# Kernel tuning notes

Measured on AMD Instinct MI355X. Metric: run time of the kernel, lower is better.

Reference implementation:

```python
import jax, jax.numpy as jnp
import numpy as np

N = 200_000      # active voxels
C_IN = 128
C_OUT = 128
GRID = 128
K = 27           # 3x3x3 submanifold kernel offsets
EPS = 1e-4       # scn BatchNormalization default eps
LEAK = 0.333     # scn LeakyReLU default leakiness


def _build_neighbor_idx(rng):
    # unique active voxel coords via unique linear keys in GRID^3
    keys = rng.choice(GRID ** 3, size=N, replace=False).astype(np.int64)
    z = keys % GRID
    y = (keys // GRID) % GRID
    x = keys // (GRID * GRID)
    coords = np.stack([x, y, z], axis=1)  # [N,3]
    order = np.argsort(keys)
    sorted_keys = keys[order]
    offs = np.array([(dx, dy, dz) for dx in (-1, 0, 1)
                     for dy in (-1, 0, 1) for dz in (-1, 0, 1)], dtype=np.int64)
    nb = np.full((N, K), -1, dtype=np.int32)
    for k in range(K):
        q = coords + offs[k]  # [N,3]
        inb = np.all((q >= 0) & (q < GRID), axis=1)
        qk = (q[:, 0] * GRID + q[:, 1]) * GRID + q[:, 2]
        pos = np.searchsorted(sorted_keys, qk)
        pos = np.clip(pos, 0, N - 1)
        hit = inb & (sorted_keys[pos] == qk)
        nb[:, k] = np.where(hit, order[pos].astype(np.int32), -1)
    return nb


def setup_inputs() -> dict:
    key = jax.random.key(0)
    k1, k2 = jax.random.split(key)
    rng = np.random.default_rng(0)
    neighbor_idx = jnp.asarray(_build_neighbor_idx(rng))       # [N,27] int32, -1 = inactive
    features = jax.random.normal(k1, (N, C_IN), dtype=jnp.float32)
    # per-offset conv weights, scn-style init scale
    W = jax.random.normal(k2, (K, C_IN, C_OUT), dtype=jnp.float32) * (1.0 / np.sqrt(K * C_IN))
    b = jnp.zeros((C_OUT,), dtype=jnp.float32)
    gamma = jnp.ones((C_OUT,), dtype=jnp.float32)
    beta = jnp.zeros((C_OUT,), dtype=jnp.float32)
    return {"features": features, "W": W, "b": b, "gamma": gamma,
            "beta": beta, "neighbor_idx": neighbor_idx}


def reference(features, W, b, gamma, beta, neighbor_idx):
    # Submanifold 3D conv: output only at active sites; gather active neighbors.
    valid = (neighbor_idx >= 0)                      # [N,27] bool
    idx = jnp.where(valid, neighbor_idx, 0)          # safe gather index
    out = jnp.broadcast_to(b, (features.shape[0], C_OUT))
    for k in range(K):  # fixed structural loop over 27 kernel offsets
        xk = features[idx[:, k]] * valid[:, k:k + 1].astype(features.dtype)  # [N,C_IN]
        out = out + xk @ W[k]                                                # [N,C_OUT]
    # BatchNormalization over all active sites (training-mode batch stats)
    mean = jnp.mean(out, axis=0)
    var = jnp.var(out, axis=0)
    out = (out - mean) * jax.lax.rsqrt(var + EPS) * gamma + beta
    # LeakyReLU (scn default leakiness 0.333)
    return jnp.where(out > 0, out, LEAK * out)
```

## Files before the change

### kernel.cpp

```cpp
#include <hip/hip_runtime.h>
#include <hip/hip_bf16.h>

#define N_VOX 200000
#define CI 128
#define CO 128
#define KK 27
#define BM 96
#define NBLK96 2084
#define NBLKFB 1563
#define NSTEP 54
#define LEAK 0.333f
#define BN_EPS 1e-4f
#define SENT 0x3FFFFu
#define ACC_STRIDE 132
#define RB_CAP 48

typedef unsigned short u16;
typedef unsigned int u32;
typedef __attribute__((ext_vector_type(8))) short short8;
typedef __attribute__((ext_vector_type(4))) float f32x4;

typedef const __attribute__((address_space(1))) u32* gptr_t;
typedef __attribute__((address_space(3))) u32* lptr_t;

__device__ __forceinline__ u16 f2bf(float f) {
  union { float f; u32 u; } x; x.f = f;
  return (u16)((x.u + 0x7FFFu + ((x.u >> 16) & 1u)) >> 16);
}
__device__ __forceinline__ u16 cvt_bf(float f) {
  union { __hip_bfloat16 h; u16 u; } c;
  c.h = __float2bfloat16(f);
  return c.u;
}
__device__ __forceinline__ int kbase_of(int k) {
  return (k < 13) ? k * RB_CAP : (k == 13 ? 13 * RB_CAP : 13 * RB_CAP + 96 + (k - 14) * RB_CAP);
}

__global__ __launch_bounds__(256) void fcast_kernel(const float* __restrict__ f,
                                                    u16* __restrict__ fb) {
  size_t i = ((size_t)blockIdx.x * 256 + threadIdx.x) * 8;
  float4 a = *(const float4*)(f + i);
  float4 b = *(const float4*)(f + i + 4);
  u16 t[8];
  t[0] = cvt_bf(a.x); t[1] = cvt_bf(a.y); t[2] = cvt_bf(a.z); t[3] = cvt_bf(a.w);
  t[4] = cvt_bf(b.x); t[5] = cvt_bf(b.y); t[6] = cvt_bf(b.z); t[7] = cvt_bf(b.w);
  *(uint4*)(fb + i) = *(const uint4*)t;
}

__global__ __launch_bounds__(256) void wcast3_kernel(const float* __restrict__ W,
                                                     u16* __restrict__ Wt3) {
  int gid = blockIdx.x * 256 + threadIdx.x;
  int lane = gid & 63, chunk = gid >> 6;
  int ks = chunk & 3, nf = (chunk >> 2) & 7, k = chunk >> 5;
  int lr = lane & 15, lg = lane >> 4;
  int co = nf * 16 + lr;
  int ci0 = ks * 32 + lg * 8;
  const float* Wk = W + (size_t)k * CI * CO;
  u16 t[8];
#pragma unroll
  for (int e = 0; e < 8; ++e) t[e] = f2bf(Wk[(ci0 + e) * CO + co]);
  *(uint4*)(Wt3 + (size_t)gid * 8) = *(const uint4*)t;
}

__global__ __launch_bounds__(256, 2) void conv_sp_kernel(
    const u16* __restrict__ featb, const u16* __restrict__ Wt3,
    const int* __restrict__ nb, const u16* __restrict__ zp,
    float* __restrict__ out, float* __restrict__ partial) {
  __shared__ __align__(16) char smem[73088];
  float* const accf = (float*)smem;
  u16* const ring = (u16*)(smem + 50688);
  u32* const rb_lds = (u32*)(smem + 67072);
  int* const cnt_lds = (int*)(smem + 72448);
  int* const wcnt = (int*)(smem + 72560);
  u32* const wl = (u32*)(smem + 72576);
  int* const wl_n = (int*)(smem + 72960);
  float* const ps = (float*)smem;

  const int tid = threadIdx.x;
  const int bid = blockIdx.x;
  const int row0 = bid * BM;
  const int lane = tid & 63;
  const int w = tid >> 6;

  {
    f32x4 z4 = {0.f, 0.f, 0.f, 0.f};
    for (int i = tid; i < (BM * ACC_STRIDE) / 4; i += 256) ((f32x4*)accf)[i] = z4;
  }

  {
    const bool inrow = (tid < BM) && (row0 + tid < N_VOX);
    const int* nbp = nb + (size_t)(row0 + tid) * KK;
    int vv[KK];
#pragma unroll
    for (int k = 0; k < KK; ++k) vv[k] = (k != 13 && inrow) ? nbp[k] : -1;
    if (tid < BM)
      rb_lds[13 * RB_CAP + tid] = ((u32)tid << 18) | (inrow ? (u32)(row0 + tid) : SENT);
    if (tid == 0) cnt_lds[13] = BM;
#pragma unroll
    for (int k = 0; k < KK; ++k) {
      if (k == 13) continue;
      bool valid = vv[k] >= 0;
      unsigned long long m = __ballot(valid);
      if (lane == 0) wcnt[w] = (int)__popcll(m);
      __syncthreads();
      int pos = (int)__popcll(m & ((1ull << lane) - 1ull)) + (w == 1 ? wcnt[0] : 0);
      int cnt = wcnt[0] + wcnt[1]; if (cnt > RB_CAP) cnt = RB_CAP;
      int kb = kbase_of(k);
      if (valid && pos < RB_CAP) rb_lds[kb + pos] = ((u32)tid << 18) | (u32)vv[k];
      int pe = (cnt + 15) & ~15;
      for (int i = cnt + tid; i < pe; i += 256) rb_lds[kb + i] = SENT;
      if (tid == 0) cnt_lds[k] = cnt;
      __syncthreads();
    }
  }

  if (tid == 0) {
    int n = 0;
    for (int k = 0; k < KK; ++k) {
      int cnt = cnt_lds[k];
      int kb = kbase_of(k);
      int ntk = (cnt + 15) >> 4;
      for (int t = 0; t < ntk; ++t) wl[n++] = ((u32)k << 11) | (u32)(kb + t * 16);
    }
    wl_n[0] = n;
  }
  __syncthreads();

  const int wv = w;
  const int lr = lane & 15, lg = lane >> 4;
  const int colbase = wv * 32 + lr;
  const int nt = wl_n[0];
  const int rt = w * 4 + (lane >> 4);
  const int pc = lane & 15;

  auto gldsA = [&](int j, int slot) {
    u32 d = wl[j];
    int off = (int)(d & 0x7FFu);
    u32 es = rb_lds[off + rt];
    u32 src = es & SENT;
    const u16* g = (src == SENT) ? zp : (featb + (size_t)src * CI);
    g += ((pc ^ rt) << 3);
    __builtin_amdgcn_global_load_lds((gptr_t)g,
        (lptr_t)(ring + slot * 2048 + w * 512), 16, 0, 0);
  };
  auto loadB = [&](int j, short8* bn) {
    int k = (int)(wl[j] >> 11);
    const u16* wb = Wt3 + (size_t)(k * 32 + wv * 8) * 512 + lane * 8;
#pragma unroll
    for (int ks = 0; ks < 4; ++ks) {
      bn[ks] = *(const short8*)(wb + ks * 512);
      bn[4 + ks] = *(const short8*)(wb + (4 + ks) * 512);
    }
  };
  auto scat4 = [&](const uint4& sc, const f32x4& c0, const f32x4& c1) {
    u32 e[4] = {sc.x, sc.y, sc.z, sc.w};
#pragma unroll
    for (int r = 0; r < 4; ++r) {
      if (e[r] != SENT) {
        int dr = (int)(e[r] >> 18);
        accf[dr * ACC_STRIDE + colbase] += c0[r];
        accf[dr * ACC_STRIDE + colbase + 16] += c1[r];
      }
    }
  };

  auto ITER = [&](int i, const short8* bcur, short8* bnext) {
    gldsA((i + 2 < nt) ? i + 2 : 0, (i + 2) & 3);
    __builtin_amdgcn_sched_barrier(0);
    loadB((i + 1 < nt) ? i + 1 : 0, bnext);
    __builtin_amdgcn_sched_barrier(0);
    asm volatile("s_waitcnt vmcnt(18)" ::: "memory");
    __builtin_amdgcn_sched_barrier(0);
    __builtin_amdgcn_s_barrier();
    __builtin_amdgcn_sched_barrier(0);
    if (i < nt) {
      u32 d = wl[i];
      int off = (int)(d & 0x7FFu);
      uint4 sc = *(const uint4*)&rb_lds[off + lg * 4];
      const u16* At = ring + (i & 3) * 2048;
      short8 a[4];
#pragma unroll
      for (int ks = 0; ks < 4; ++ks) {
        int p = (ks * 4 + lg) ^ lr;
        a[ks] = *(const short8*)(At + lr * 128 + p * 8);
      }
      f32x4 c0 = {0.f, 0.f, 0.f, 0.f}, c1 = {0.f, 0.f, 0.f, 0.f};
#pragma unroll
      for (int ks = 0; ks < 4; ++ks) {
        c0 = __builtin_amdgcn_mfma_f32_16x16x32_bf16(a[ks], bcur[ks], c0, 0, 0, 0);
        c1 = __builtin_amdgcn_mfma_f32_16x16x32_bf16(a[ks], bcur[4 + ks], c1, 0, 0, 0);
      }
      scat4(sc, c0, c1);
    }
    __builtin_amdgcn_sched_barrier(0);
  };

  {
    short8 b0v[8], b1v[8];
    gldsA(0, 0);
    gldsA(1, 1);
    loadB(0, b0v);
    __builtin_amdgcn_sched_barrier(0);
    for (int i = 0; i < nt; i += 2) {
      ITER(i, b0v, b1v);
      ITER(i + 1, b1v, b0v);
    }
  }
  __syncthreads();

  float s4[4] = {0.f, 0.f, 0.f, 0.f}, q4[4] = {0.f, 0.f, 0.f, 0.f};
  const int col4 = (tid & 31) * 4;
  const int rgrp = tid >> 5;
#pragma unroll
  for (int i = 0; i < 12; ++i) {
    int row = rgrp + i * 8;
    f32x4 v = *(const f32x4*)&accf[row * ACC_STRIDE + col4];
    int grow = row0 + row;
    if (grow < N_VOX) {
      *(float4*)&out[(size_t)grow * CO + col4] = *(float4*)&v;
#pragma unroll
      for (int j = 0; j < 4; ++j) { s4[j] += v[j]; q4[j] += v[j] * v[j]; }
    }
  }
  __syncthreads();
#pragma unroll
  for (int j = 0; j < 4; ++j) {
    ps[rgrp * 128 + col4 + j] = s4[j];
    ps[1024 + rgrp * 128 + col4 + j] = q4[j];
  }
  __syncthreads();
  {
    int col = tid & 127, which = tid >> 7;
    float acc = 0.f;
#pragma unroll
    for (int g = 0; g < 8; ++g) acc += ps[which * 1024 + g * 128 + col];
    partial[(size_t)bid * 256 + tid] = acc;
  }
}

__global__ __launch_bounds__(256, 2) void conv_fb_kernel(
    const float* __restrict__ feat, const u16* __restrict__ Wt3,
    const int* __restrict__ nb, float* __restrict__ out,
    float* __restrict__ partial) {
  __shared__ __align__(16) char smem[46592];
  u16* const Ab = (u16*)smem;
  int* const nbs = (int*)(smem + 32768);
  float* const sq = (float*)smem;

  const int tid = threadIdx.x;
  const int bid = blockIdx.x;
  const int row0 = bid * 128;

  for (int i = tid; i < 128 * KK; i += 256) {
    int gi = row0 * KK + i;
    nbs[i] = (gi < N_VOX * KK) ? nb[gi] : -1;
  }
  __syncthreads();

  const int lane = tid & 63;
  const int wv = tid >> 6;
  const int wr = wv >> 1, wc = wv & 1;
  const int lr = lane & 15, lg = lane >> 4;
  const int arow = tid >> 1;
  const int acol = (tid & 1) * 32;

  f32x4 acc[4][4];
#pragma unroll
  for (int m = 0; m < 4; ++m)
#pragma unroll
    for (int n = 0; n < 4; ++n) acc[m][n] = (f32x4){0.f, 0.f, 0.f, 0.f};

  float4 af[8];
  short8 b0[8], b1[8];

  auto issueAf = [&](int s) {
    int k = s >> 1, half = (s & 1) * 64;
    int src = nbs[arow * KK + k];
    if (src >= 0) {
      const float4* p = (const float4*)(feat + (size_t)src * CI + half + acol);
#pragma unroll
      for (int j = 0; j < 8; ++j) af[j] = p[j];
    } else {
#pragma unroll
      for (int j = 0; j < 8; ++j) af[j] = (float4){0.f, 0.f, 0.f, 0.f};
    }
  };
  auto loadB = [&](int s, short8* bn) {
    int k = s >> 1, half = s & 1;
#pragma unroll
    for (int n = 0; n < 4; ++n)
#pragma unroll
      for (int ks = 0; ks < 2; ++ks)
        bn[n * 2 + ks] = *(const short8*)(Wt3 +
            (size_t)((k * 32 + (wc * 4 + n) * 4) + half * 2 + ks) * 512 + lane * 8);
  };
  auto writeA = [&](u16* Adst) {
    int v = arow & 7;
#pragma unroll
    for (int q = 0; q < 4; ++q) {
      u16 t8[8];
#pragma unroll
      for (int i = 0; i < 2; ++i) {
        float4 f = af[q * 2 + i];
        t8[i * 4 + 0] = cvt_bf(f.x); t8[i * 4 + 1] = cvt_bf(f.y);
        t8[i * 4 + 2] = cvt_bf(f.z); t8[i * 4 + 3] = cvt_bf(f.w);
      }
      int c_o = (tid & 1) * 4 + q;
      *(uint4*)&Adst[arow * 64 + ((c_o ^ v) << 3)] = *(const uint4*)t8;
    }
  };
  auto compute = [&](const u16* A, const short8* bc) {
#pragma unroll
    for (int ks = 0; ks < 2; ++ks) {
      short8 a[4];
#pragma unroll
      for (int m = 0; m < 4; ++m) {
        int r = wr * 64 + m * 16 + lr;
        a[m] = *(const short8*)((const char*)A + r * 128 +
                                ((ks * 64 + lg * 16) ^ ((r & 7) << 4)));
      }
#pragma unroll
      for (int m = 0; m < 4; ++m)
#pragma unroll
        for (int n = 0; n < 4; ++n)
          acc[m][n] = __builtin_amdgcn_mfma_f32_16x16x32_bf16(a[m], bc[n * 2 + ks],
                                                              acc[m][n], 0, 0, 0);
    }
  };

  issueAf(0);
  loadB(0, b0);
  for (int s = 0; s + 2 <= NSTEP - 1; s += 2) {
    writeA(Ab + (s & 1) * 8192); __syncthreads();
    issueAf(s + 1); loadB(s + 1, b1);
    compute(Ab + (s & 1) * 8192, b0);
    writeA(Ab + ((s + 1) & 1) * 8192); __syncthreads();
    issueAf(s + 2); loadB(s + 2, b0);
    compute(Ab + ((s + 1) & 1) * 8192, b1);
  }
  writeA(Ab); __syncthreads();
  issueAf(NSTEP - 1); loadB(NSTEP - 1, b1);
  compute(Ab, b0);
  writeA(Ab + 8192); __syncthreads();
  compute(Ab + 8192, b1);

  float sv[4], qv[4];
#pragma unroll
  for (int n = 0; n < 4; ++n) {
    float s = 0.f, q = 0.f;
    int col = wc * 64 + n * 16 + lr;
#pragma unroll
    for (int m = 0; m < 4; ++m) {
      int rb_ = row0 + wr * 64 + m * 16 + lg * 4;
#pragma unroll
      for (int e = 0; e < 4; ++e) {
        float x = acc[m][n][e];
        if (rb_ + e < N_VOX) out[(size_t)(rb_ + e) * CO + col] = x;
        s += x; q += x * x;
      }
    }
    s += __shfl_xor(s, 16, 64); s += __shfl_xor(s, 32, 64);
    q += __shfl_xor(q, 16, 64); q += __shfl_xor(q, 32, 64);
    sv[n] = s; qv[n] = q;
  }
  __syncthreads();
  if (lg == 0) {
#pragma unroll
    for (int n = 0; n < 4; ++n) {
      int col = wc * 64 + n * 16 + lr;
      sq[wr * 256 + col] = sv[n];
      sq[wr * 256 + 128 + col] = qv[n];
    }
  }
  __syncthreads();
  partial[(size_t)bid * 256 + tid] = sq[tid] + sq[256 + tid];
}

__global__ __launch_bounds__(256) void reduce1_kernel(const float* __restrict__ partial,
                                                      float* __restrict__ partial2,
                                                      int nblk) {
  int t = threadIdx.x, b = blockIdx.x;
  float acc = 0.f;
  int jend = (b + 1) * 16; if (jend > nblk) jend = nblk;
  for (int j = b * 16; j < jend; ++j) acc += partial[(size_t)j * 256 + t];
  partial2[(size_t)b * 256 + t] = acc;
}

__global__ __launch_bounds__(256) void reduce2_kernel(const float* __restrict__ partial2,
                                                      const float* __restrict__ gamma,
                                                      const float* __restrict__ beta,
                                                      float* __restrict__ stats, int n2) {
  __shared__ float sums[256];
  int t = threadIdx.x;
  float acc = 0.f;
  for (int j = 0; j < n2; ++j) acc += partial2[(size_t)j * 256 + t];
  sums[t] = acc;
  __syncthreads();
  if (t < 128) {
    float mean = sums[t] / (float)N_VOX;
    float var = sums[128 + t] / (float)N_VOX - mean * mean;
    float scale = gamma[t] * rsqrtf(var + BN_EPS);
    stats[t] = scale;
    stats[128 + t] = beta[t] - mean * scale;
  }
}

__global__ __launch_bounds__(256) void bnact_kernel(float* __restrict__ out,
                                                    const float* __restrict__ stats) {
  __shared__ float s_scale[128], s_shift[128];
  int t = threadIdx.x;
  if (t < 128) { s_scale[t] = stats[t]; s_shift[t] = stats[128 + t]; }
  __syncthreads();
  size_t i = (size_t)blockIdx.x * 256 + t;
  float4* o4 = (float4*)out;
  float4 v = o4[i];
  int c0 = ((int)(i & 31)) << 2;
  float x;
  x = v.x * s_scale[c0 + 0] + s_shift[c0 + 0]; v.x = x > 0.f ? x : LEAK * x;
  x = v.y * s_scale[c0 + 1] + s_shift[c0 + 1]; v.y = x > 0.f ? x : LEAK * x;
  x = v.z * s_scale[c0 + 2] + s_shift[c0 + 2]; v.z = x > 0.f ? x : LEAK * x;
  x = v.w * s_scale[c0 + 3] + s_shift[c0 + 3]; v.w = x > 0.f ? x : LEAK * x;
  o4[i] = v;
}

extern "C" void kernel_launch(void* const* d_in, const int* in_sizes, int n_in,
                              void* d_out, int out_size, void* d_ws, size_t ws_size,
                              hipStream_t stream) {
  const float* feat  = (const float*)d_in[0];
  const float* W     = (const float*)d_in[1];
  const float* gamma = (const float*)d_in[3];
  const float* beta  = (const float*)d_in[4];
  const int*   nb    = (const int*)d_in[5];
  float* out = (float*)d_out;

  char* ws = (char*)d_ws;
  u16*   Wt3      = (u16*)ws;
  float* partial  = (float*)(ws + 884736);
  float* partial2 = (float*)(ws + 3018752);
  float* stats    = (float*)(ws + 3152896);
  u16*   zp       = (u16*)(ws + 3153920);
  u16*   featb    = (u16*)(ws + 3154176);
  const size_t need_fast = 54354176u;

  hipLaunchKernelGGL(wcast3_kernel, dim3(216), dim3(256), 0, stream, W, Wt3);
  if (ws_size >= need_fast) {
    hipMemsetAsync(zp, 0, 256, stream);
    hipLaunchKernelGGL(fcast_kernel, dim3(12500), dim3(256), 0, stream, feat, featb);
    hipLaunchKernelGGL(conv_sp_kernel, dim3(NBLK96), dim3(256), 0, stream,
                       featb, Wt3, nb, zp, out, partial);
    hipLaunchKernelGGL(reduce1_kernel, dim3(131), dim3(256), 0, stream,
                       partial, partial2, NBLK96);
    hipLaunchKernelGGL(reduce2_kernel, dim3(1), dim3(256), 0, stream,
                       partial2, gamma, beta, stats, 131);
  } else {
    hipLaunchKernelGGL(conv_fb_kernel, dim3(NBLKFB), dim3(256), 0, stream,
                       feat, Wt3, nb, out, partial);
    hipLaunchKernelGGL(reduce1_kernel, dim3(98), dim3(256), 0, stream,
                       partial, partial2, NBLKFB);
    hipLaunchKernelGGL(reduce2_kernel, dim3(1), dim3(256), 0, stream,
                       partial2, gamma, beta, stats, 98);
  }
  hipLaunchKernelGGL(bnact_kernel, dim3(25000), dim3(256), 0, stream, out, stats);
}
```

Before: 298.2 us.

## Store LDS accumulator in bf16 and load A tiles directly to registers

The per-block fp32 LDS accumulator becomes a bf16 accumulator, and the LDS ring buffer fed by global_load_lds is removed in favour of direct global-to-register A loads. Together these cut shared memory from about 73 KB to about 31 KB, and launch bounds rise to 4 blocks per CU to raise occupancy. The software pipeline with its explicit barriers is replaced by a simpler loop over paired tiles, with a padding tile added when the tile count is odd. Accumulating 27 partial sums in bf16 with rounding at every step loses significant precision and may break tolerance.

Measured after the change: 291.3 us. 2.3% less time.

```diff
diff --git a/kernel.cpp b/kernel.cpp
--- a/kernel.cpp
+++ b/kernel.cpp
@@ -14,6 +14,7 @@
 #define SENT 0x3FFFFu
 #define ACC_STRIDE 132
 #define RB_CAP 48
+#define RB_PAD 1344
 
 typedef unsigned short u16;
 typedef unsigned int u32;
@@ -27,13 +28,17 @@
   union { float f; u32 u; } x; x.f = f;
   return (u16)((x.u + 0x7FFFu + ((x.u >> 16) & 1u)) >> 16);
 }
+__device__ __forceinline__ float bf2f(u16 h) {
+  union { u32 u; float f; } x; x.u = ((u32)h) << 16;
+  return x.f;
+}
 __device__ __forceinline__ u16 cvt_bf(float f) {
   union { __hip_bfloat16 h; u16 u; } c;
   c.h = __float2bfloat16(f);
   return c.u;
 }
 __device__ __forceinline__ int kbase_of(int k) {
-  return (k < 13) ? k * RB_CAP : (k == 13 ? 13 * RB_CAP : 13 * RB_CAP + 96 + (k - 14) * RB_CAP);
+  return (k < 13) ? k * RB_CAP : (k == 13 ? 13 * RB_CAP : 13 * RB_CAP + BM + (k - 14) * RB_CAP);
 }
 
 __global__ __launch_bounds__(256) void fcast_kernel(const float* __restrict__ f,
@@ -62,18 +67,17 @@
   *(uint4*)(Wt3 + (size_t)gid * 8) = *(const uint4*)t;
 }
 
-__global__ __launch_bounds__(256, 2) void conv_sp_kernel(
+__global__ __launch_bounds__(256, 4) void conv_sp_kernel(
     const u16* __restrict__ featb, const u16* __restrict__ Wt3,
     const int* __restrict__ nb, const u16* __restrict__ zp,
     float* __restrict__ out, float* __restrict__ partial) {
-  __shared__ __align__(16) char smem[73088];
-  float* const accf = (float*)smem;
-  u16* const ring = (u16*)(smem + 50688);
-  u32* const rb_lds = (u32*)(smem + 67072);
-  int* const cnt_lds = (int*)(smem + 72448);
-  int* const wcnt = (int*)(smem + 72560);
-  u32* const wl = (u32*)(smem + 72576);
-  int* const wl_n = (int*)(smem + 72960);
+  __shared__ __align__(16) char smem[31312];
+  u16* const accb = (u16*)smem;
+  u32* const rb_lds = (u32*)(smem + 25344);
+  int* const cnt_lds = (int*)(smem + 30784);
+  int* const wcnt = (int*)(smem + 30896);
+  u32* const wl = (u32*)(smem + 30912);
+  int* const wl_n = (int*)(smem + 31296);
   float* const ps = (float*)smem;
 
   const int tid = threadIdx.x;
@@ -82,10 +86,8 @@
   const int lane = tid & 63;
   const int w = tid >> 6;
 
-  {
-    f32x4 z4 = {0.f, 0.f, 0.f, 0.f};
-    for (int i = tid; i < (BM * ACC_STRIDE) / 4; i += 256) ((f32x4*)accf)[i] = z4;
-  }
+  for (int i = tid; i < (BM * ACC_STRIDE) / 2; i += 256) ((u32*)accb)[i] = 0u;
+  if (tid < 16) rb_lds[RB_PAD + tid] = SENT;
 
   {
     const bool inrow = (tid < BM) && (row0 + tid < N_VOX);
@@ -122,6 +124,7 @@
       int ntk = (cnt + 15) >> 4;
       for (int t = 0; t < ntk; ++t) wl[n++] = ((u32)k << 11) | (u32)(kb + t * 16);
     }
+    if (n & 1) wl[n++] = (u32)RB_PAD;
     wl_n[0] = n;
   }
   __syncthreads();
@@ -130,81 +133,52 @@
   const int lr = lane & 15, lg = lane >> 4;
   const int colbase = wv * 32 + lr;
   const int nt = wl_n[0];
-  const int rt = w * 4 + (lane >> 4);
-  const int pc = lane & 15;
-
-  auto gldsA = [&](int j, int slot) {
-    u32 d = wl[j];
+
+  auto loadTile = [&](u32 d, uint4& sc, short8* a) {
     int off = (int)(d & 0x7FFu);
-    u32 es = rb_lds[off + rt];
+    u32 es = rb_lds[off + lr];
+    sc = *(const uint4*)&rb_lds[off + lg * 4];
     u32 src = es & SENT;
-    const u16* g = (src == SENT) ? zp : (featb + (size_t)src * CI);
-    g += ((pc ^ rt) << 3);
-    __builtin_amdgcn_global_load_lds((gptr_t)g,
-        (lptr_t)(ring + slot * 2048 + w * 512), 16, 0, 0);
-  };
-  auto loadB = [&](int j, short8* bn) {
-    int k = (int)(wl[j] >> 11);
+    const u16* ap = (src == SENT) ? zp : (featb + (size_t)src * CI);
+#pragma unroll
+    for (int ks = 0; ks < 4; ++ks) a[ks] = *(const short8*)(ap + ks * 32 + lg * 8);
+  };
+  auto loadB = [&](u32 d, short8* b) {
+    int k = (int)(d >> 11);
     const u16* wb = Wt3 + (size_t)(k * 32 + wv * 8) * 512 + lane * 8;
 #pragma unroll
+    for (int j = 0; j < 8; ++j) b[j] = *(const short8*)(wb + j * 512);
+  };
+  auto mfma_scat = [&](const short8* a, const short8* b, const uint4& sc) {
+    f32x4 c0 = {0.f, 0.f, 0.f, 0.f}, c1 = {0.f, 0.f, 0.f, 0.f};
+#pragma unroll
     for (int ks = 0; ks < 4; ++ks) {
-      bn[ks] = *(const short8*)(wb + ks * 512);
-      bn[4 + ks] = *(const short8*)(wb + (4 + ks) * 512);
-    }
-  };
-  auto scat4 = [&](const uint4& sc, const f32x4& c0, const f32x4& c1) {
+      c0 = __builtin_amdgcn_mfma_f32_16x16x32_bf16(a[ks], b[ks], c0, 0, 0, 0);
+      c1 = __builtin_amdgcn_mfma_f32_16x16x32_bf16(a[ks], b[4 + ks], c1, 0, 0, 0);
+    }
     u32 e[4] = {sc.x, sc.y, sc.z, sc.w};
 #pragma unroll
     for (int r = 0; r < 4; ++r) {
       if (e[r] != SENT) {
-        int dr = (int)(e[r] >> 18);
-        accf[dr * ACC_STRIDE + colbase] += c0[r];
-        accf[dr * ACC_STRIDE + colbase + 16] += c1[r];
+        int i0 = (int)(e[r] >> 18) * ACC_STRIDE + colbase;
+        accb[i0] = f2bf(bf2f(accb[i0]) + c0[r]);
+        accb[i0 + 16] = f2bf(bf2f(accb[i0 + 16]) + c1[r]);
       }
     }
   };
 
-  auto ITER = [&](int i, const short8* bcur, short8* bnext) {
-    gldsA((i + 2 < nt) ? i + 2 : 0, (i + 2) & 3);
+  for (int i = 0; i < nt; i += 2) {
+    u32 d0 = wl[i], d1 = wl[i + 1];
+    uint4 sc0, sc1;
+    short8 a0[4], a1[4], b0[8], b1[8];
+    loadTile(d0, sc0, a0);
+    loadTile(d1, sc1, a1);
+    loadB(d0, b0);
     __builtin_amdgcn_sched_barrier(0);
-    loadB((i + 1 < nt) ? i + 1 : 0, bnext);
+    mfma_scat(a0, b0, sc0);
+    loadB(d1, b1);
     __builtin_amdgcn_sched_barrier(0);
-    asm volatile("s_waitcnt vmcnt(18)" ::: "memory");
-    __builtin_amdgcn_sched_barrier(0);
-    __builtin_amdgcn_s_barrier();
-    __builtin_amdgcn_sched_barrier(0);
-    if (i < nt) {
-      u32 d = wl[i];
-      int off = (int)(d & 0x7FFu);
-      uint4 sc = *(const uint4*)&rb_lds[off + lg * 4];
-      const u16* At = ring + (i & 3) * 2048;
-      short8 a[4];
-#pragma unroll
-      for (int ks = 0; ks < 4; ++ks) {
-        int p = (ks * 4 + lg) ^ lr;
-        a[ks] = *(const short8*)(At + lr * 128 + p * 8);
-      }
-      f32x4 c0 = {0.f, 0.f, 0.f, 0.f}, c1 = {0.f, 0.f, 0.f, 0.f};
-#pragma unroll
-      for (int ks = 0; ks < 4; ++ks) {
-        c0 = __builtin_amdgcn_mfma_f32_16x16x32_bf16(a[ks], bcur[ks], c0, 0, 0, 0);
-        c1 = __builtin_amdgcn_mfma_f32_16x16x32_bf16(a[ks], bcur[4 + ks], c1, 0, 0, 0);
-      }
-      scat4(sc, c0, c1);
-    }
-    __builtin_amdgcn_sched_barrier(0);
-  };
-
-  {
-    short8 b0v[8], b1v[8];
-    gldsA(0, 0);
-    gldsA(1, 1);
-    loadB(0, b0v);
-    __builtin_amdgcn_sched_barrier(0);
-    for (int i = 0; i < nt; i += 2) {
-      ITER(i, b0v, b1v);
-      ITER(i + 1, b1v, b0v);
-    }
+    mfma_scat(a1, b1, sc1);
   }
   __syncthreads();
 
@@ -214,12 +188,16 @@
 #pragma unroll
   for (int i = 0; i < 12; ++i) {
     int row = rgrp + i * 8;
-    f32x4 v = *(const f32x4*)&accf[row * ACC_STRIDE + col4];
+    const u16* ap = &accb[row * ACC_STRIDE + col4];
+    float4 v;
+    v.x = bf2f(ap[0]); v.y = bf2f(ap[1]); v.z = bf2f(ap[2]); v.w = bf2f(ap[3]);
     int grow = row0 + row;
     if (grow < N_VOX) {
-      *(float4*)&out[(size_t)grow * CO + col4] = *(float4*)&v;
-#pragma unroll
-      for (int j = 0; j < 4; ++j) { s4[j] += v[j]; q4[j] += v[j] * v[j]; }
+      *(float4*)&out[(size_t)grow * CO + col4] = v;
+      s4[0] += v.x; q4[0] += v.x * v.x;
+      s4[1] += v.y; q4[1] += v.y * v.y;
+      s4[2] += v.z; q4[2] += v.z * v.z;
+      s4[3] += v.w; q4[3] += v.w * v.w;
     }
   }
   __syncthreads();
```
